# Kernel optimization log

Measured on AMD Instinct MI355X. Metric: run time of the kernel, lower is better.

Reference implementation:

```python
import jax, jax.numpy as jnp
import numpy as np

STRIDES = (8, 16, 32, 64, 128)
SCORE_THRESH = 0.05
IOU_THRESH = 0.6
MAX_DET = 1000


def _flat(p):
    # [B,C,H,W] -> [B,H*W,C]
    B, C = p.shape[0], p.shape[1]
    return jnp.transpose(p, (0, 2, 3, 1)).reshape(B, -1, C)


def _coords(h, w, stride):
    # FCOS coords_fmap2orig: center of each stride cell, (x, y) order -> [h*w, 2]
    sx = (jnp.arange(w, dtype=jnp.float32) * stride + stride // 2)
    sy = (jnp.arange(h, dtype=jnp.float32) * stride + stride // 2)
    yy, xx = jnp.meshgrid(sy, sx, indexing='ij')
    return jnp.stack([xx.ravel(), yy.ravel()], axis=-1)


def _nms_keep(boxes, valid, thr):
    # boxes: [M,4] sorted by descending score; valid: [M] bool. Greedy NMS keep mask.
    x1, y1, x2, y2 = boxes[:, 0], boxes[:, 1], boxes[:, 2], boxes[:, 3]
    area = (x2 - x1 + 1.0) * (y2 - y1 + 1.0)
    xx1 = jnp.maximum(x1[:, None], x1[None, :])
    yy1 = jnp.maximum(y1[:, None], y1[None, :])
    xx2 = jnp.minimum(x2[:, None], x2[None, :])
    yy2 = jnp.minimum(y2[:, None], y2[None, :])
    inter = jnp.clip(xx2 - xx1, 0.0) * jnp.clip(yy2 - yy1, 0.0)
    iou = inter / (area[:, None] + area[None, :] - inter)
    M = boxes.shape[0]
    idx = jnp.arange(M)

    def body(i, keep):
        sup = (idx > i) & (iou[i] > thr) & keep[i]
        return keep & (~sup)

    return jax.lax.fori_loop(0, M, body, valid)


def setup_inputs() -> dict:
    key = jax.random.key(0)
    B, C = 16, 80
    sizes = [(128, 128), (64, 64), (32, 32), (16, 16), (8, 8)]
    ks = jax.random.split(key, 15)
    inp = {}
    for i, (h, w) in enumerate(sizes):
        lvl = i + 3
        inp[f'cls_p{lvl}'] = jax.random.normal(ks[3 * i], (B, C, h, w), jnp.float32)
        inp[f'cnt_p{lvl}'] = jax.random.normal(ks[3 * i + 1], (B, 1, h, w), jnp.float32)
        inp[f'reg_p{lvl}'] = jax.random.uniform(ks[3 * i + 2], (B, 4, h, w), jnp.float32) * 100.0
    return inp


def _detect(cls_levels, cnt_levels, reg_levels):
    cls_logits = jnp.concatenate([_flat(p) for p in cls_levels], axis=1)  # [B,N,80]
    cnt_logits = jnp.concatenate([_flat(p) for p in cnt_levels], axis=1)  # [B,N,1]
    reg_preds = jnp.concatenate([_flat(p) for p in reg_levels], axis=1)   # [B,N,4]
    coords = jnp.concatenate(
        [_coords(p.shape[2], p.shape[3], s) for p, s in zip(cls_levels, STRIDES)], axis=0)  # [N,2]

    cls_preds = jax.nn.sigmoid(cls_logits)
    cnt_preds = jax.nn.sigmoid(cnt_logits)[..., 0]                        # [B,N]
    cls_max = jnp.max(cls_preds, axis=-1)                                 # [B,N]
    cls_classes = jnp.argmax(cls_preds, axis=-1) + 1                      # [B,N] 1-based labels
    scores = jnp.sqrt(cls_max * cnt_preds)                                # add_centerness

    boxes = jnp.concatenate(
        [coords[None] - reg_preds[..., :2], coords[None] + reg_preds[..., 2:]], axis=-1)  # [B,N,4]

    M = min(MAX_DET, scores.shape[1])
    topv, topi = jax.lax.top_k(scores, M)                                 # sorted desc
    classes_k = jnp.take_along_axis(cls_classes, topi, axis=1)            # [B,M]
    boxes_k = jnp.take_along_axis(boxes, topi[..., None], axis=1)         # [B,M,4]
    valid = topv >= SCORE_THRESH

    def per_image(b, s, c, v):
        # class-aware NMS via coordinate offset trick
        off = c.astype(b.dtype) * (jnp.max(b) + 1.0)
        keep = _nms_keep(b + off[:, None], v, IOU_THRESH)
        kf = keep.astype(s.dtype)
        return s * kf, c * keep.astype(c.dtype), b * kf[:, None]

    return jax.vmap(per_image)(boxes_k, topv, classes_k, valid)


def reference(cls_p3, cnt_p3, reg_p3, cls_p4, cnt_p4, reg_p4, cls_p5, cnt_p5, reg_p5,
              cls_p6, cnt_p6, reg_p6, cls_p7, cnt_p7, reg_p7):
    cls_levels = [cls_p3, cls_p4, cls_p5, cls_p6, cls_p7]
    cnt_levels = [cnt_p3, cnt_p4, cnt_p5, cnt_p6, cnt_p7]
    reg_levels = [reg_p3, reg_p4, reg_p5, reg_p6, reg_p7]
    return _detect(cls_levels, cnt_levels, reg_levels)
```

## Files before the change

kernel.cpp:

```cpp
#include <hip/hip_runtime.h>
#include <math.h>

#define NB 16
#define NC 80
#define NA 21824
#define NM 1000
#define NHBINS 2048
#define CANDCAP 4096
#define BSZ 1024

#define OFF_KEYS     0ul
#define OFF_CLSV     2793472ul
#define OFF_TOPSCORE 4190208ul
#define OFF_TOPCLS   4254208ul
#define OFF_TOPBOX   4318208ul
#define OFF_MAXB     4574208ul
#define OFF_MASK     4574272ul

__device__ __forceinline__ float sigm(float x) { return 1.0f / (1.0f + expf(-x)); }

__global__ __launch_bounds__(256, 6) void k_score(
    const float* __restrict__ cls3, const float* __restrict__ cnt3,
    const float* __restrict__ cls4, const float* __restrict__ cnt4,
    const float* __restrict__ cls5, const float* __restrict__ cnt5,
    const float* __restrict__ cls6, const float* __restrict__ cnt6,
    const float* __restrict__ cls7, const float* __restrict__ cnt7,
    unsigned long long* __restrict__ keys,
    float* __restrict__ clsv)
{
    __shared__ float lm[4 * 64 * 4];
    __shared__ int   lam[4 * 64 * 4];
    __shared__ float cm[256];
    __shared__ int   cam[256];
    const int b = blockIdx.y;
    const int tid = threadIdx.x;
    const int a = tid & 63, s = tid >> 6;
    const int g4 = blockIdx.x * 64 + a;

    if (g4 < (NA >> 2)) {
        const int n = g4 << 2;
        const float* clsP; int off, logW;
        if      (n < 16384) { clsP = cls3; off = 0;     logW = 7; }
        else if (n < 20480) { clsP = cls4; off = 16384; logW = 6; }
        else if (n < 21504) { clsP = cls5; off = 20480; logW = 5; }
        else if (n < 21760) { clsP = cls6; off = 21504; logW = 4; }
        else                { clsP = cls7; off = 21760; logW = 3; }
        const int HW4 = 1 << (2 * logW - 2);
        const int l4 = (n - off) >> 2;
        const float4* cp = (const float4*)clsP + (size_t)b * NC * HW4 + l4;
        const int c0 = s * 20;
        float4 buf[4];
#pragma unroll
        for (int u = 0; u < 4; u++) buf[u] = cp[(size_t)(c0 + u) * HW4];
        float m[4] = { -3.402823466e+38f, -3.402823466e+38f, -3.402823466e+38f, -3.402823466e+38f };
        int am[4] = { c0, c0, c0, c0 };
#pragma unroll
        for (int u = 0; u < 20; u++) {
            float4 vv = buf[u & 3];
            if (u + 4 < 20) buf[u & 3] = cp[(size_t)(c0 + u + 4) * HW4];
            const int c = c0 + u;
            if (vv.x > m[0]) { m[0] = vv.x; am[0] = c; }
            if (vv.y > m[1]) { m[1] = vv.y; am[1] = c; }
            if (vv.z > m[2]) { m[2] = vv.z; am[2] = c; }
            if (vv.w > m[3]) { m[3] = vv.w; am[3] = c; }
        }
#pragma unroll
        for (int k = 0; k < 4; k++) { lm[tid * 4 + k] = m[k]; lam[tid * 4 + k] = am[k]; }
    }
    __syncthreads();
    if (tid < 64 && (blockIdx.x * 64 + tid) < (NA >> 2)) {
        float M[4]; int AM[4];
#pragma unroll
        for (int k = 0; k < 4; k++) { M[k] = lm[tid * 4 + k]; AM[k] = lam[tid * 4 + k]; }
        for (int s2 = 1; s2 < 4; s2++) {
#pragma unroll
            for (int k = 0; k < 4; k++) {
                float vv = lm[(s2 * 64 + tid) * 4 + k];
                if (vv > M[k]) { M[k] = vv; AM[k] = lam[(s2 * 64 + tid) * 4 + k]; }
            }
        }
#pragma unroll
        for (int k = 0; k < 4; k++) { cm[tid * 4 + k] = M[k]; cam[tid * 4 + k] = AM[k]; }
    }
    __syncthreads();
    const int n2 = blockIdx.x * 256 + tid;
    if (n2 < NA) {
        const float* cntP; int off, logW;
        if      (n2 < 16384) { cntP = cnt3; off = 0;     logW = 7; }
        else if (n2 < 20480) { cntP = cnt4; off = 16384; logW = 6; }
        else if (n2 < 21504) { cntP = cnt5; off = 20480; logW = 5; }
        else if (n2 < 21760) { cntP = cnt6; off = 21504; logW = 4; }
        else                 { cntP = cnt7; off = 21760; logW = 3; }
        const int HW = 1 << (2 * logW);
        const int local = n2 - off;
        float cn = cntP[(size_t)b * HW + local];
        float M = cm[tid]; int AM = cam[tid];
        float sc = sqrtf(sigm(M) * sigm(cn));
        unsigned long long key = ((unsigned long long)__float_as_uint(sc) << 32)
                               | (unsigned int)(~(unsigned int)n2);
        keys[(size_t)b * NA + n2] = key;
        clsv[(size_t)b * NA + n2] = (float)(AM + 1);
    }
}

__global__ __launch_bounds__(BSZ) void k_mid(
    const unsigned long long* __restrict__ keys, const float* __restrict__ clsv,
    const float* __restrict__ reg3, const float* __restrict__ reg4, const float* __restrict__ reg5,
    const float* __restrict__ reg6, const float* __restrict__ reg7,
    float* __restrict__ topscore, float* __restrict__ topcls,
    float4* __restrict__ topbox, float* __restrict__ maxb)
{
    __shared__ unsigned int sh_hist[NHBINS];
    __shared__ unsigned int sh_cur[NHBINS];
    __shared__ unsigned int sh_off[NHBINS];
    __shared__ unsigned int sh_subh[NHBINS];
    __shared__ unsigned int sh_subo[NHBINS];
    __shared__ unsigned int sh_subc[NHBINS];
    __shared__ unsigned long long scand[NM];
    __shared__ unsigned long long scand2[CANDCAP];
    __shared__ int part1[BSZ];
    __shared__ int part2[32];
    __shared__ int sBoundary;
    __shared__ float redmax[BSZ];

    const int b = blockIdx.x;
    const int tid = threadIdx.x;
    const ulonglong2* k2 = (const ulonglong2*)(keys + (size_t)b * NA);

    for (int i = tid; i < NHBINS; i += BSZ) {
        sh_hist[i] = 0u; sh_cur[i] = 0u; sh_subh[i] = 0u; sh_subc[i] = 0u;
    }
    __syncthreads();

    for (int i = tid; i < NA / 2; i += BSZ) {
        ulonglong2 v = k2[i];
        atomicAdd(&sh_hist[(unsigned int)(v.x >> 51)], 1u);
        atomicAdd(&sh_hist[(unsigned int)(v.y >> 51)], 1u);
    }
    __syncthreads();

    part1[tid] = (int)sh_hist[2 * tid] + (int)sh_hist[2 * tid + 1];
    __syncthreads();
    if (tid < 32) { int s2 = 0; for (int t = 0; t < 32; t++) s2 += part1[tid * 32 + t]; part2[tid] = s2; }
    __syncthreads();

    if (tid == 0) {
        int acc = 0, g;
        for (g = 31; g > 0; g--) { if (acc + part2[g] >= NM) break; acc += part2[g]; }
        int t;
        for (t = g * 32 + 31; t > g * 32; t--) { if (acc + part1[t] >= NM) break; acc += part1[t]; }
        int bin = 2 * t + 1;
        if (acc + (int)sh_hist[bin] < NM) { acc += (int)sh_hist[bin]; bin = 2 * t; }
        sBoundary = bin;
    }
    {
        const int g = tid >> 5;
        int acc = 0;
        for (int q = g + 1; q < 32; q++) acc += part2[q];
        for (int t2 = (g << 5) + 31; t2 > tid; t2--) acc += part1[t2];
        sh_off[2 * tid + 1] = (unsigned int)acc;
        sh_off[2 * tid]     = (unsigned int)(acc + (int)sh_hist[2 * tid + 1]);
    }
    __syncthreads();

    const unsigned int boundary = (unsigned int)sBoundary;
    const int s0 = (int)sh_off[boundary];

    for (int i = tid; i < NA / 2; i += BSZ) {
        ulonglong2 v = k2[i];
#pragma unroll
        for (int h = 0; h < 2; h++) {
            const unsigned long long kk = h ? v.y : v.x;
            const unsigned int bb = (unsigned int)(kk >> 51);
            if (bb > boundary) {
                unsigned int p = sh_off[bb] + atomicAdd(&sh_cur[bb], 1u);
                if (p < (unsigned int)NM) scand[p] = kk;
            } else if (bb == boundary) {
                atomicAdd(&sh_subh[(unsigned int)(kk >> 40) & 2047u], 1u);
            }
        }
    }
    __syncthreads();

    part1[tid] = (int)sh_subh[2 * tid] + (int)sh_subh[2 * tid + 1];
    __syncthreads();
    if (tid < 32) { int s2 = 0; for (int t = 0; t < 32; t++) s2 += part1[tid * 32 + t]; part2[tid] = s2; }
    __syncthreads();
    {
        const int g = tid >> 5;
        int acc = 0;
        for (int q = g + 1; q < 32; q++) acc += part2[q];
        for (int t2 = (g << 5) + 31; t2 > tid; t2--) acc += part1[t2];
        sh_subo[2 * tid + 1] = (unsigned int)acc;
        sh_subo[2 * tid]     = (unsigned int)(acc + (int)sh_subh[2 * tid + 1]);
    }
    __syncthreads();

    for (int i = tid; i < NA / 2; i += BSZ) {
        ulonglong2 v = k2[i];
#pragma unroll
        for (int h = 0; h < 2; h++) {
            const unsigned long long kk = h ? v.y : v.x;
            if ((unsigned int)(kk >> 51) == boundary) {
                unsigned int sb = (unsigned int)(kk >> 40) & 2047u;
                unsigned int p = sh_subo[sb] + atomicAdd(&sh_subc[sb], 1u);
                if (p < CANDCAP) scand2[p] = kk;
            }
        }
    }
    __syncthreads();

    int Lbs = (int)sh_hist[boundary]; if (Lbs > CANDCAP) Lbs = CANDCAP;
    const int cnt = s0 + Lbs;
    float mymax = -3.402823466e+38f;
    for (int idx = tid; idx < cnt; idx += BSZ) {
        unsigned long long key; int rank;
        if (idx < s0) {
            key = scand[idx];
            const unsigned int bin = (unsigned int)(key >> 51);
            int g0 = (int)sh_off[bin];
            int g1 = g0 + (int)sh_hist[bin]; if (g1 > s0) g1 = s0;
            rank = g0;
            for (int j = g0; j < g1; j++) rank += (scand[j] > key);
        } else {
            key = scand2[idx - s0];
            const unsigned int sb = (unsigned int)(key >> 40) & 2047u;
            int t0 = (int)sh_subo[sb];
            int t1 = t0 + (int)sh_subh[sb]; if (t1 > Lbs) t1 = Lbs;
            rank = s0 + t0;
            for (int j = t0; j < t1; j++) rank += (scand2[j] > key);
        }
        if (rank < NM) {
            const unsigned int ai = ~(unsigned int)key;
            const float* regP; int lvloff, W, logW, st;
            if      (ai < 16384) { regP = reg3; lvloff = 0;     W = 128; logW = 7; st = 8;   }
            else if (ai < 20480) { regP = reg4; lvloff = 16384; W = 64;  logW = 6; st = 16;  }
            else if (ai < 21504) { regP = reg5; lvloff = 20480; W = 32;  logW = 5; st = 32;  }
            else if (ai < 21760) { regP = reg6; lvloff = 21504; W = 16;  logW = 4; st = 64;  }
            else                 { regP = reg7; lvloff = 21760; W = 8;   logW = 3; st = 128; }
            const int local = (int)ai - lvloff;
            const int HW = 1 << (2 * logW);
            const float* rp = regP + (size_t)b * 4 * HW + local;
            float r0 = rp[0], r1 = rp[HW], r2 = rp[2 * HW], r3 = rp[3 * HW];
            float cv = clsv[(size_t)b * NA + ai];
            const float hs = (float)(st >> 1);
            float cx = (float)((local & (W - 1)) * st) + hs;
            float cy = (float)((local >> logW) * st) + hs;
            float4 bxv = make_float4(cx - r0, cy - r1, cx + r2, cy + r3);
            topscore[b * NM + rank] = __uint_as_float((unsigned int)(key >> 32));
            topcls[b * NM + rank] = cv;
            topbox[b * NM + rank] = bxv;
            mymax = fmaxf(mymax, fmaxf(fmaxf(bxv.x, bxv.y), fmaxf(bxv.z, bxv.w)));
        }
    }
    redmax[tid] = mymax;
    __syncthreads();
    for (int sgap = BSZ / 2; sgap > 0; sgap >>= 1) {
        if (tid < sgap) redmax[tid] = fmaxf(redmax[tid], redmax[tid + sgap]);
        __syncthreads();
    }
    if (tid == 0) maxb[b] = __fadd_rn(redmax[0], 1.0f);
}

__global__ __launch_bounds__(256) void k_iou(
    const float4* __restrict__ topbox, const float* __restrict__ topcls,
    const float* __restrict__ maxb, unsigned long long* __restrict__ maskArr)
{
    __shared__ float4 sB[NM];
    __shared__ float sA[NM];
    const int b = blockIdx.y;
    const int tid = threadIdx.x;
    const float mp1 = maxb[b];
    for (int r = tid; r < NM; r += 256) {
        float4 f = topbox[b * NM + r];
        float off = __fmul_rn(topcls[b * NM + r], mp1);
        f.x = __fadd_rn(f.x, off); f.y = __fadd_rn(f.y, off);
        f.z = __fadd_rn(f.z, off); f.w = __fadd_rn(f.w, off);
        sB[r] = f;
        sA[r] = __fmul_rn(__fadd_rn(__fsub_rn(f.z, f.x), 1.0f),
                          __fadd_rn(__fsub_rn(f.w, f.y), 1.0f));
    }
    __syncthreads();
    int task = blockIdx.x * 256 + tid;
    if (task >= NM * 16) return;
    int w = task / NM, i = task - w * NM;
    float4 bi = sB[i]; float ai = sA[i];
    unsigned long long bits = 0ULL;
    int j0 = w << 6;
    int jstart = (j0 > i + 1) ? j0 : i + 1;
    int jend = (j0 + 64 < NM) ? j0 + 64 : NM;
    for (int j = jstart; j < jend; j++) {
        float4 bj = sB[j];
        float xx1 = fmaxf(bi.x, bj.x);
        float yy1 = fmaxf(bi.y, bj.y);
        float xx2 = fminf(bi.z, bj.z);
        float yy2 = fminf(bi.w, bj.w);
        float iw = fmaxf(__fsub_rn(xx2, xx1), 0.0f);
        float ih = fmaxf(__fsub_rn(yy2, yy1), 0.0f);
        float inter = __fmul_rn(iw, ih);
        float denom = __fsub_rn(__fadd_rn(ai, sA[j]), inter);
        float iou = inter / denom;
        if (iou > 0.6f) bits |= (1ULL << (j - j0));
    }
    maskArr[((size_t)b * 16 + w) * NM + i] = bits;
}

__global__ __launch_bounds__(256) void k_nms_sweep(
    const unsigned long long* __restrict__ maskArr,
    const float* __restrict__ topscore, const float* __restrict__ topcls,
    const float4* __restrict__ topbox, float* __restrict__ out)
{
    __shared__ unsigned long long smask[16 * NM];
    __shared__ unsigned long long lremv[16];
    const int b = blockIdx.x;
    const int tid = threadIdx.x;
    const int j = tid & 63, q = tid >> 6;
    const unsigned long long* gmask = maskArr + (size_t)b * (16 * NM);

    {
        const ulonglong2* src = (const ulonglong2*)gmask;
        ulonglong2* dst = (ulonglong2*)smask;
        for (int idx = tid; idx < 8 * NM; idx += 256) dst[idx] = src[idx];
    }
    if (tid < 16) lremv[tid] = 0ULL;
    __syncthreads();
    for (int r = tid; r < NM; r += 256) {
        float s = topscore[b * NM + r];
        if (!(s >= 0.05f)) atomicOr(&lremv[r >> 6], 1ULL << (r & 63));
    }

    for (int w = 0; w < 16; w++) {
        __syncthreads();
        const int row = w * 64 + j;
        unsigned long long D = (row < NM) ? smask[w * NM + row] : 0ULL;
        unsigned int dlo = (unsigned int)D, dhi = (unsigned int)(D >> 32);
        unsigned long long sv = lremv[w];
        unsigned int slo = __builtin_amdgcn_readfirstlane((unsigned int)sv);
        unsigned int shi = __builtin_amdgcn_readfirstlane((unsigned int)(sv >> 32));
        unsigned long long s = ((unsigned long long)shi << 32) | slo;
#pragma unroll
        for (int bb = 0; bb < 64; bb++) {
            unsigned int rlo = __builtin_amdgcn_readlane(dlo, bb);
            unsigned int rhi = __builtin_amdgcn_readlane(dhi, bb);
            unsigned long long rowv = ((unsigned long long)rhi << 32) | rlo;
            unsigned long long t = s | rowv;
            s = ((s >> bb) & 1ULL) ? s : t;
        }
        if (tid == 0) lremv[w] = s;
        const unsigned long long kw = ~s;
        if ((kw >> j) & 1ULL) {
            for (int k = w + 1 + q; k < 16; k += 4) {
                unsigned long long v = (row < NM) ? smask[k * NM + row] : 0ULL;
                if (v) atomicOr(&lremv[k], v);
            }
        }
    }
    __syncthreads();

    for (int r = tid; r < NM; r += 256) {
        bool keep = !((lremv[r >> 6] >> (r & 63)) & 1ULL);
        float kf = keep ? 1.0f : 0.0f;
        out[b * NM + r] = topscore[b * NM + r] * kf;
        out[NB * NM + b * NM + r] = topcls[b * NM + r] * kf;
        float4 bx = topbox[b * NM + r];
        ((float4*)(out + 2 * NB * NM))[b * NM + r] = make_float4(bx.x * kf, bx.y * kf, bx.z * kf, bx.w * kf);
    }
}

extern "C" void kernel_launch(void* const* d_in, const int* in_sizes, int n_in,
                              void* d_out, int out_size, void* d_ws, size_t ws_size,
                              hipStream_t stream) {
    const float* cls3 = (const float*)d_in[0];
    const float* cnt3 = (const float*)d_in[1];
    const float* reg3 = (const float*)d_in[2];
    const float* cls4 = (const float*)d_in[3];
    const float* cnt4 = (const float*)d_in[4];
    const float* reg4 = (const float*)d_in[5];
    const float* cls5 = (const float*)d_in[6];
    const float* cnt5 = (const float*)d_in[7];
    const float* reg5 = (const float*)d_in[8];
    const float* cls6 = (const float*)d_in[9];
    const float* cnt6 = (const float*)d_in[10];
    const float* reg6 = (const float*)d_in[11];
    const float* cls7 = (const float*)d_in[12];
    const float* cnt7 = (const float*)d_in[13];
    const float* reg7 = (const float*)d_in[14];

    char* ws = (char*)d_ws;
    unsigned long long* keys   = (unsigned long long*)(ws + OFF_KEYS);
    float*              clsv   = (float*)(ws + OFF_CLSV);
    float*              topsc  = (float*)(ws + OFF_TOPSCORE);
    float*              topcl  = (float*)(ws + OFF_TOPCLS);
    float4*             topbx  = (float4*)(ws + OFF_TOPBOX);
    float*              maxbF  = (float*)(ws + OFF_MAXB);
    unsigned long long* maskA  = (unsigned long long*)(ws + OFF_MASK);

    dim3 g1(86, NB);
    k_score<<<g1, 256, 0, stream>>>(cls3, cnt3, cls4, cnt4, cls5, cnt5,
                                    cls6, cnt6, cls7, cnt7,
                                    keys, clsv);
    k_mid<<<dim3(NB), BSZ, 0, stream>>>(keys, clsv, reg3, reg4, reg5, reg6, reg7,
                                        topsc, topcl, topbx, maxbF);
    dim3 g4(63, NB);
    k_iou<<<g4, 256, 0, stream>>>(topbx, topcl, maxbF, maskA);
    k_nms_sweep<<<NB, 256, 0, stream>>>(maskA, topsc, topcl, topbx, (float*)d_out);
}
```

Baseline: 265.4 us.

## Fuse top-k, IoU mask and NMS sweep into one per-image kernel

Merges the selection, IoU bitmask and greedy sweep kernels into a single 1024-thread block per image. Top-k scores, classes and boxes stay in LDS, and the IoU mask aliases the histogram scratch space. This removes two launches and the global round trips for the mask and top-k arrays. In exchange, the IoU mask computation now runs on only 16 blocks instead of about a thousand, so it may become a serial bottleneck.

```diff
diff --git a/kernel.cpp b/kernel.cpp
--- a/kernel.cpp
+++ b/kernel.cpp
@@ -11,11 +11,7 @@
 
 #define OFF_KEYS     0ul
 #define OFF_CLSV     2793472ul
-#define OFF_TOPSCORE 4190208ul
-#define OFF_TOPCLS   4254208ul
-#define OFF_TOPBOX   4318208ul
-#define OFF_MAXB     4574208ul
-#define OFF_MASK     4574272ul
+#define OFF_TOPBOX   4190208ul
 
 __device__ __forceinline__ float sigm(float x) { return 1.0f / (1.0f + expf(-x)); }
 
@@ -103,25 +99,34 @@
     }
 }
 
-__global__ __launch_bounds__(BSZ) void k_mid(
+__global__ __launch_bounds__(BSZ, 1) void k_fused(
     const unsigned long long* __restrict__ keys, const float* __restrict__ clsv,
     const float* __restrict__ reg3, const float* __restrict__ reg4, const float* __restrict__ reg5,
     const float* __restrict__ reg6, const float* __restrict__ reg7,
-    float* __restrict__ topscore, float* __restrict__ topcls,
-    float4* __restrict__ topbox, float* __restrict__ maxb)
+    float4* __restrict__ gbox,
+    float* __restrict__ out)
 {
-    __shared__ unsigned int sh_hist[NHBINS];
-    __shared__ unsigned int sh_cur[NHBINS];
-    __shared__ unsigned int sh_off[NHBINS];
-    __shared__ unsigned int sh_subh[NHBINS];
-    __shared__ unsigned int sh_subo[NHBINS];
-    __shared__ unsigned int sh_subc[NHBINS];
-    __shared__ unsigned long long scand[NM];
-    __shared__ unsigned long long scand2[CANDCAP];
-    __shared__ int part1[BSZ];
-    __shared__ int part2[32];
-    __shared__ int sBoundary;
-    __shared__ float redmax[BSZ];
+    __shared__ float  stopsc[NM];
+    __shared__ float  stopcl[NM];
+    __shared__ float4 stopbx[NM];
+    __shared__ float  sA[NM];
+    __shared__ unsigned long long lremv[16];
+    __shared__ float  smaxb;
+    __shared__ int    sBoundary;
+    __shared__ alignas(16) unsigned char un[16 * NM * 8];
+
+    unsigned int* sh_hist = (unsigned int*)(un);
+    unsigned int* sh_cur  = (unsigned int*)(un + 8192);
+    unsigned int* sh_off  = (unsigned int*)(un + 16384);
+    unsigned int* sh_subh = (unsigned int*)(un + 24576);
+    unsigned int* sh_subo = (unsigned int*)(un + 32768);
+    unsigned int* sh_subc = (unsigned int*)(un + 40960);
+    unsigned long long* scand  = (unsigned long long*)(un + 49152);
+    unsigned long long* scand2 = (unsigned long long*)(un + 57344);
+    int*   part1  = (int*)(un + 90112);
+    int*   part2  = (int*)(un + 94208);
+    float* redmax = (float*)(un + 94336);
+    unsigned long long* smask = (unsigned long long*)(un);
 
     const int b = blockIdx.x;
     const int tid = threadIdx.x;
@@ -247,9 +252,10 @@
             float cx = (float)((local & (W - 1)) * st) + hs;
             float cy = (float)((local >> logW) * st) + hs;
             float4 bxv = make_float4(cx - r0, cy - r1, cx + r2, cy + r3);
-            topscore[b * NM + rank] = __uint_as_float((unsigned int)(key >> 32));
-            topcls[b * NM + rank] = cv;
-            topbox[b * NM + rank] = bxv;
+            stopsc[rank] = __uint_as_float((unsigned int)(key >> 32));
+            stopcl[rank] = cv;
+            stopbx[rank] = bxv;
+            gbox[b * NM + rank] = bxv;
             mymax = fmaxf(mymax, fmaxf(fmaxf(bxv.x, bxv.y), fmaxf(bxv.z, bxv.w)));
         }
     }
@@ -259,76 +265,49 @@
         if (tid < sgap) redmax[tid] = fmaxf(redmax[tid], redmax[tid + sgap]);
         __syncthreads();
     }
-    if (tid == 0) maxb[b] = __fadd_rn(redmax[0], 1.0f);
-}
-
-__global__ __launch_bounds__(256) void k_iou(
-    const float4* __restrict__ topbox, const float* __restrict__ topcls,
-    const float* __restrict__ maxb, unsigned long long* __restrict__ maskArr)
-{
-    __shared__ float4 sB[NM];
-    __shared__ float sA[NM];
-    const int b = blockIdx.y;
-    const int tid = threadIdx.x;
-    const float mp1 = maxb[b];
-    for (int r = tid; r < NM; r += 256) {
-        float4 f = topbox[b * NM + r];
-        float off = __fmul_rn(topcls[b * NM + r], mp1);
+    if (tid == 0) smaxb = __fadd_rn(redmax[0], 1.0f);
+    __syncthreads();
+
+    const float mp1 = smaxb;
+    for (int r = tid; r < NM; r += BSZ) {
+        float4 f = stopbx[r];
+        float off = __fmul_rn(stopcl[r], mp1);
         f.x = __fadd_rn(f.x, off); f.y = __fadd_rn(f.y, off);
         f.z = __fadd_rn(f.z, off); f.w = __fadd_rn(f.w, off);
-        sB[r] = f;
+        stopbx[r] = f;
         sA[r] = __fmul_rn(__fadd_rn(__fsub_rn(f.z, f.x), 1.0f),
                           __fadd_rn(__fsub_rn(f.w, f.y), 1.0f));
     }
-    __syncthreads();
-    int task = blockIdx.x * 256 + tid;
-    if (task >= NM * 16) return;
-    int w = task / NM, i = task - w * NM;
-    float4 bi = sB[i]; float ai = sA[i];
-    unsigned long long bits = 0ULL;
-    int j0 = w << 6;
-    int jstart = (j0 > i + 1) ? j0 : i + 1;
-    int jend = (j0 + 64 < NM) ? j0 + 64 : NM;
-    for (int j = jstart; j < jend; j++) {
-        float4 bj = sB[j];
-        float xx1 = fmaxf(bi.x, bj.x);
-        float yy1 = fmaxf(bi.y, bj.y);
-        float xx2 = fminf(bi.z, bj.z);
-        float yy2 = fminf(bi.w, bj.w);
-        float iw = fmaxf(__fsub_rn(xx2, xx1), 0.0f);
-        float ih = fmaxf(__fsub_rn(yy2, yy1), 0.0f);
-        float inter = __fmul_rn(iw, ih);
-        float denom = __fsub_rn(__fadd_rn(ai, sA[j]), inter);
-        float iou = inter / denom;
-        if (iou > 0.6f) bits |= (1ULL << (j - j0));
-    }
-    maskArr[((size_t)b * 16 + w) * NM + i] = bits;
-}
-
-__global__ __launch_bounds__(256) void k_nms_sweep(
-    const unsigned long long* __restrict__ maskArr,
-    const float* __restrict__ topscore, const float* __restrict__ topcls,
-    const float4* __restrict__ topbox, float* __restrict__ out)
-{
-    __shared__ unsigned long long smask[16 * NM];
-    __shared__ unsigned long long lremv[16];
-    const int b = blockIdx.x;
-    const int tid = threadIdx.x;
+    if (tid < 16) lremv[tid] = 0ULL;
+    __syncthreads();
+
+    for (int task = tid; task < NM * 16; task += BSZ) {
+        int w = task / NM, i = task - w * NM;
+        float4 bi = stopbx[i]; float ai = sA[i];
+        unsigned long long bits = 0ULL;
+        int j0 = w << 6;
+        int jstart = (j0 > i + 1) ? j0 : i + 1;
+        int jend = (j0 + 64 < NM) ? j0 + 64 : NM;
+        for (int j = jstart; j < jend; j++) {
+            float4 bj = stopbx[j];
+            float xx1 = fmaxf(bi.x, bj.x);
+            float yy1 = fmaxf(bi.y, bj.y);
+            float xx2 = fminf(bi.z, bj.z);
+            float yy2 = fminf(bi.w, bj.w);
+            float iw = fmaxf(__fsub_rn(xx2, xx1), 0.0f);
+            float ih = fmaxf(__fsub_rn(yy2, yy1), 0.0f);
+            float inter = __fmul_rn(iw, ih);
+            float denom = __fsub_rn(__fadd_rn(ai, sA[j]), inter);
+            float iou = inter / denom;
+            if (iou > 0.6f) bits |= (1ULL << (j - j0));
+        }
+        smask[w * NM + i] = bits;
+    }
+    for (int r = tid; r < NM; r += BSZ) {
+        if (!(stopsc[r] >= 0.05f)) atomicOr(&lremv[r >> 6], 1ULL << (r & 63));
+    }
+
     const int j = tid & 63, q = tid >> 6;
-    const unsigned long long* gmask = maskArr + (size_t)b * (16 * NM);
-
-    {
-        const ulonglong2* src = (const ulonglong2*)gmask;
-        ulonglong2* dst = (ulonglong2*)smask;
-        for (int idx = tid; idx < 8 * NM; idx += 256) dst[idx] = src[idx];
-    }
-    if (tid < 16) lremv[tid] = 0ULL;
-    __syncthreads();
-    for (int r = tid; r < NM; r += 256) {
-        float s = topscore[b * NM + r];
-        if (!(s >= 0.05f)) atomicOr(&lremv[r >> 6], 1ULL << (r & 63));
-    }
-
     for (int w = 0; w < 16; w++) {
         __syncthreads();
         const int row = w * 64 + j;
@@ -349,7 +328,8 @@
         if (tid == 0) lremv[w] = s;
         const unsigned long long kw = ~s;
         if ((kw >> j) & 1ULL) {
-            for (int k = w + 1 + q; k < 16; k += 4) {
+            int k = w + 1 + q;
+            if (k < 16) {
                 unsigned long long v = (row < NM) ? smask[k * NM + row] : 0ULL;
                 if (v) atomicOr(&lremv[k], v);
             }
@@ -357,12 +337,12 @@
     }
     __syncthreads();
 
-    for (int r = tid; r < NM; r += 256) {
+    for (int r = tid; r < NM; r += BSZ) {
         bool keep = !((lremv[r >> 6] >> (r & 63)) & 1ULL);
         float kf = keep ? 1.0f : 0.0f;
-        out[b * NM + r] = topscore[b * NM + r] * kf;
-        out[NB * NM + b * NM + r] = topcls[b * NM + r] * kf;
-        float4 bx = topbox[b * NM + r];
+        out[b * NM + r] = stopsc[r] * kf;
+        out[NB * NM + b * NM + r] = stopcl[r] * kf;
+        float4 bx = gbox[b * NM + r];
         ((float4*)(out + 2 * NB * NM))[b * NM + r] = make_float4(bx.x * kf, bx.y * kf, bx.z * kf, bx.w * kf);
     }
 }
@@ -387,21 +367,14 @@
     const float* reg7 = (const float*)d_in[14];
 
     char* ws = (char*)d_ws;
-    unsigned long long* keys   = (unsigned long long*)(ws + OFF_KEYS);
-    float*              clsv   = (float*)(ws + OFF_CLSV);
-    float*              topsc  = (float*)(ws + OFF_TOPSCORE);
-    float*              topcl  = (float*)(ws + OFF_TOPCLS);
-    float4*             topbx  = (float4*)(ws + OFF_TOPBOX);
-    float*              maxbF  = (float*)(ws + OFF_MAXB);
-    unsigned long long* maskA  = (unsigned long long*)(ws + OFF_MASK);
+    unsigned long long* keys = (unsigned long long*)(ws + OFF_KEYS);
+    float*              clsv = (float*)(ws + OFF_CLSV);
+    float4*             gbox = (float4*)(ws + OFF_TOPBOX);
 
     dim3 g1(86, NB);
     k_score<<<g1, 256, 0, stream>>>(cls3, cnt3, cls4, cnt4, cls5, cnt5,
                                     cls6, cnt6, cls7, cnt7,
                                     keys, clsv);
-    k_mid<<<dim3(NB), BSZ, 0, stream>>>(keys, clsv, reg3, reg4, reg5, reg6, reg7,
-                                        topsc, topcl, topbx, maxbF);
-    dim3 g4(63, NB);
-    k_iou<<<g4, 256, 0, stream>>>(topbx, topcl, maxbF, maskA);
-    k_nms_sweep<<<NB, 256, 0, stream>>>(maskA, topsc, topcl, topbx, (float*)d_out);
+    k_fused<<<dim3(NB), BSZ, 0, stream>>>(keys, clsv, reg3, reg4, reg5, reg6, reg7,
+                                          gbox, (float*)d_out);
 }
```

Result: slower. 406.4 us (+53.2%).
